# Kernel optimization log

Hardware: AMD Instinct MI355X
Metric: run time of the kernel (lower is better)

## Reference

```python
import jax, jax.numpy as jnp
import numpy as np

DIM = 256; HEADS = 8; HD = 32; WS = 3; LOCAL = WS * WS; SR = 4


def _unfold(x, ws):
    # x: (B, c, H, W) -> (B, c, ws*ws, H*W), zero padding (matches nn.Unfold)
    p = ws // 2
    B, c, H, W = x.shape
    xp = jnp.pad(x, ((0, 0), (0, 0), (p, p), (p, p)))
    pat = jnp.stack([xp[:, :, i:i + H, j:j + W] for i in range(ws) for j in range(ws)], axis=2)
    return pat.reshape(B, c, ws * ws, H * W)


def _l2norm(x):
    return x / jnp.sqrt(jnp.sum(x * x, axis=-1, keepdims=True) + 1e-12)


def setup_inputs():
    key = jax.random.key(0)
    ks = jax.random.split(key, 16)
    B, H, W, C, h, d = 4, 64, 64, DIM, HEADS, HD
    N = H * W; pH, pW = H // SR, W // SR; PL = pH * pW; L = 1024
    s = 0.02
    inp = {}
    inp["x"] = jax.random.normal(ks[0], (B, N, C), jnp.float32)
    inp["relative_coords_table"] = jax.random.uniform(ks[1], (L, 2), jnp.float32, -1.0, 1.0)
    inp["relative_pos_index"] = jax.random.randint(ks[2], (N, PL), 0, L)
    inp["q_w"] = jax.random.normal(ks[3], (C, C), jnp.float32) * s
    inp["q_b"] = jnp.zeros((C,), jnp.float32)
    inp["kv_w"] = jax.random.normal(ks[4], (C, 2 * C), jnp.float32) * s
    inp["kv_b"] = jnp.zeros((2 * C,), jnp.float32)
    inp["temperature"] = jnp.log(jnp.expm1(jnp.ones((h, 1, 1), jnp.float32) / 0.24))
    inp["query_embedding"] = jax.random.normal(ks[5], (h, 1, d), jnp.float32) * s
    inp["sr_w"] = jax.random.normal(ks[6], (C, C), jnp.float32) * s
    inp["sr_b"] = jnp.zeros((C,), jnp.float32)
    inp["norm_g"] = jnp.ones((C,), jnp.float32)
    inp["norm_b"] = jnp.zeros((C,), jnp.float32)
    inp["cpb1_w"] = jax.random.normal(ks[7], (2, 512), jnp.float32) * s
    inp["cpb1_b"] = jnp.zeros((512,), jnp.float32)
    inp["cpb2_w"] = jax.random.normal(ks[8], (512, h), jnp.float32) * s
    inp["cpb2_b"] = jnp.zeros((h,), jnp.float32)
    inp["rpb_local"] = jax.random.normal(ks[9], (h, LOCAL), jnp.float32) * 0.0004
    inp["learnable_tokens"] = jax.random.normal(ks[10], (h, d, LOCAL), jnp.float32) * s
    inp["learnable_bias"] = jnp.zeros((h, 1, LOCAL), jnp.float32)
    inp["proj_w"] = jax.random.normal(ks[11], (C, C), jnp.float32) * s
    inp["proj_b"] = jnp.zeros((C,), jnp.float32)
    inp["H"] = H
    inp["W"] = W
    return inp


def _forward(x, relative_coords_table, relative_pos_index, q_w, q_b, kv_w, kv_b,
             temperature, query_embedding, sr_w, sr_b, norm_g, norm_b,
             cpb1_w, cpb1_b, cpb2_w, cpb2_b, rpb_local, learnable_tokens,
             learnable_bias, proj_w, proj_b, H, W):
    B, N, C = x.shape
    h, d = HEADS, HD
    pH, pW = H // SR, W // SR
    PL = pH * pW

    # static buffers: per-pixel valid-neighbor count, log seq-length scale, padding mask
    uf1 = _unfold(jnp.ones((1, 1, H, W), jnp.float32), WS)[0, 0]   # (LOCAL, N)
    counts = uf1.sum(axis=0)[:, None]                               # (N, 1)
    seq_scale = jnp.log(counts + PL)                                # (N, 1)
    pad_mask = (uf1.T == 0)                                         # (N, LOCAL)

    q = (x @ q_w + q_b).reshape(B, N, h, d).transpose(0, 2, 1, 3)   # (B,h,N,d)
    q_norm = _l2norm(q)
    q_scaled = (q_norm + query_embedding) * jax.nn.softplus(temperature) * seq_scale

    kv = (x @ kv_w + kv_b).reshape(B, N, 2 * h, d).transpose(0, 2, 1, 3)
    k_local, v_local = kv[:, :h], kv[:, h:]                         # (B,h,N,d)

    # --- local branch: sliding-window QK^T + learned relative bias ---
    kn = _l2norm(k_local)
    k_img = kn.transpose(0, 1, 3, 2).reshape(B, h * d, H, W)
    k_uf = _unfold(k_img, WS).reshape(B, h, d, LOCAL, N)            # (B,h,d,l,N)
    attn_local = jnp.einsum('bhnd,bhdln->bhnl', q_scaled, k_uf) + rpb_local[None, :, None, :]
    attn_local = jnp.where(pad_mask[None, None], jnp.float32(-1e9), attn_local)

    # --- pooled global branch ---
    xs = jax.nn.gelu(x @ sr_w + sr_b, approximate=False)            # 1x1 conv + GELU
    xs = xs.reshape(B, pH, SR, pW, SR, C).mean(axis=(2, 4)).reshape(B, PL, C)
    mu = xs.mean(-1, keepdims=True)
    var = ((xs - mu) ** 2).mean(-1, keepdims=True)
    xs = (xs - mu) / jnp.sqrt(var + 1e-5) * norm_g + norm_b         # LayerNorm

    kvp = (xs @ kv_w + kv_b).reshape(B, PL, 2 * h, d).transpose(0, 2, 1, 3)
    k_pool, v_pool = kvp[:, :h], kvp[:, h:]
    kp = _l2norm(k_pool)

    # MLP-generated continuous relative position bias
    t = jax.nn.relu(relative_coords_table @ cpb1_w + cpb1_b) @ cpb2_w + cpb2_b  # (L,h)
    pool_bias = t.T[:, relative_pos_index.reshape(-1)].reshape(h, N, PL)

    attn_pool = jnp.einsum('bhnd,bhpd->bhnp', q_scaled, kp) + pool_bias[None]

    # joint softmax over [local | pool]
    attn = jax.nn.softmax(jnp.concatenate([attn_local, attn_pool], axis=-1), axis=-1)
    attn_local, attn_pool = attn[..., :LOCAL], attn[..., LOCAL:]

    # learnable-token refinement of local weights
    attn_local = jnp.einsum('bhnd,hdl->bhnl', q_norm, learnable_tokens) + learnable_bias[None] + attn_local

    v_img = v_local.transpose(0, 1, 3, 2).reshape(B, h * d, H, W)
    v_uf = _unfold(v_img, WS).reshape(B, h, d, LOCAL, N)            # zero-padded V
    x_local = jnp.einsum('bhnl,bhdln->bhnd', attn_local, v_uf)
    x_pool = jnp.einsum('bhnp,bhpd->bhnd', attn_pool, v_pool)

    out = (x_local + x_pool).transpose(0, 2, 1, 3).reshape(B, N, C)
    return out @ proj_w + proj_b


def reference(x, relative_coords_table, relative_pos_index, q_w, q_b, kv_w, kv_b,
              temperature, query_embedding, sr_w, sr_b, norm_g, norm_b,
              cpb1_w, cpb1_b, cpb2_w, cpb2_b, rpb_local, learnable_tokens,
              learnable_bias, proj_w, proj_b, H, W):
    return _forward(x, relative_coords_table, relative_pos_index, q_w, q_b, kv_w, kv_b,
                    temperature, query_embedding, sr_w, sr_b, norm_g, norm_b,
                    cpb1_w, cpb1_b, cpb2_w, cpb2_b, rpb_local, learnable_tokens,
                    learnable_bias, proj_w, proj_b, H, W)
```

## Files before the change

### kernel.cpp

```cpp
#include <hip/hip_runtime.h>
#include <math.h>

#define B_   4
#define N_   4096
#define C_   256
#define NH   8
#define D_   32
#define PL_  256
#define IMG  64

typedef __attribute__((ext_vector_type(8))) short short8b;
typedef __attribute__((ext_vector_type(4))) float f32x4;
typedef unsigned short ushort_t;

__device__ __forceinline__ ushort_t f2bf(float f) {
    unsigned u = __float_as_uint(f);
    u += 0x7FFFu + ((u >> 16) & 1u);
    return (ushort_t)(u >> 16);
}
__device__ __forceinline__ float bf2f(ushort_t s) {
    return __uint_as_float(((unsigned)s) << 16);
}
__device__ __forceinline__ unsigned pk2(float lo, float hi) {
    return (unsigned)f2bf(lo) | ((unsigned)f2bf(hi) << 16);
}
__device__ __forceinline__ float gelu_f(float v) {
    return 0.5f * v * (1.0f + erff(v * 0.70710678118654752440f));
}

__global__ __launch_bounds__(256) void prep_w(const float* __restrict__ x,
                                              const float* __restrict__ q_w,
                                              const float* __restrict__ kv_w,
                                              const float* __restrict__ sr_w,
                                              const float* __restrict__ p_w,
                                              ushort_t* __restrict__ x_bf,
                                              ushort_t* __restrict__ WTall,
                                              ushort_t* __restrict__ pwT)
{
    int gid = blockIdx.x * 256 + threadIdx.x;
    if (gid < 524288) {
        const float4* p = (const float4*)(x + (size_t)gid * 8);
        float4 v0 = p[0], v1 = p[1];
        short8b o;
        o[0]=(short)f2bf(v0.x); o[1]=(short)f2bf(v0.y);
        o[2]=(short)f2bf(v0.z); o[3]=(short)f2bf(v0.w);
        o[4]=(short)f2bf(v1.x); o[5]=(short)f2bf(v1.y);
        o[6]=(short)f2bf(v1.z); o[7]=(short)f2bf(v1.w);
        *(short8b*)&x_bf[(size_t)gid * 8] = o;
    } else {
        int wt = gid - 524288;
        int row = wt >> 5;
        int k0  = (wt & 31) << 3;
        const float* W; int N, n; ushort_t* dst;
        if (row < 256)       { W = q_w;  N = 256; n = row;        dst = WTall + (size_t)row * 256; }
        else if (row < 768)  { W = kv_w; N = 512; n = row - 256;  dst = WTall + (size_t)row * 256; }
        else if (row < 1024) { W = sr_w; N = 256; n = row - 768;  dst = WTall + (size_t)row * 256; }
        else                 { W = p_w;  N = 256; n = row - 1024; dst = pwT + (size_t)(row-1024) * 256; }
        short8b v;
        #pragma unroll
        for (int j = 0; j < 8; ++j) v[j] = (short)f2bf(W[(size_t)(k0 + j) * N + n]);
        *(short8b*)&dst[k0] = v;
    }
}

__global__ __launch_bounds__(256) void gemm_fused(const ushort_t* __restrict__ Abf,
                                                  const ushort_t* __restrict__ WTall,
                                                  const float* __restrict__ q_b,
                                                  const float* __restrict__ kv_b,
                                                  const float* __restrict__ sr_b,
                                                  float* __restrict__ buf_q,
                                                  float* __restrict__ buf_kv,
                                                  float* __restrict__ buf_sr)
{
    __shared__ __align__(16) ushort_t Bs[64 * 256];

    const int tid  = threadIdx.x;
    const int wv   = tid >> 6;
    const int lane = tid & 63;
    const int la   = lane & 15, lg = lane >> 4;
    const int m0   = blockIdx.y * 128 + wv * 32;
    const int bx   = blockIdx.x;
    const int n0   = bx * 64;

    {
        const int srow = tid >> 2, sm = tid & 3;
        const ushort_t* wrow = WTall + (size_t)(n0 + srow) * 256;
        #pragma unroll
        for (int c8 = 0; c8 < 8; ++c8) {
            int ck = c8 * 4 + sm;
            short8b v = *(const short8b*)&wrow[ck * 8];
            *(short8b*)&Bs[srow * 256 + ((ck ^ (srow & 3)) * 8)] = v;
        }
    }
    __syncthreads();

    const ushort_t* a0p = Abf + (size_t)(m0 + la) * 256 + lg * 8;
    const ushort_t* a1p = a0p + (size_t)16 * 256;

    f32x4 acc[2][4];
    #pragma unroll
    for (int i = 0; i < 2; ++i)
        #pragma unroll
        for (int j = 0; j < 4; ++j) acc[i][j] = (f32x4){0.f, 0.f, 0.f, 0.f};

    #pragma unroll
    for (int kit = 0; kit < 8; ++kit) {
        short8b a0 = *(const short8b*)(a0p + kit * 32);
        short8b a1 = *(const short8b*)(a1p + kit * 32);
        #pragma unroll
        for (int nf = 0; nf < 4; ++nf) {
            int brow = nf * 16 + la;
            short8b bb = *(const short8b*)&Bs[brow * 256 + (((kit*4 + lg) ^ (la & 3)) * 8)];
            acc[0][nf] = __builtin_amdgcn_mfma_f32_16x16x32_bf16(a0, bb, acc[0][nf], 0, 0, 0);
            acc[1][nf] = __builtin_amdgcn_mfma_f32_16x16x32_bf16(a1, bb, acc[1][nf], 0, 0, 0);
        }
    }

    float* outp; const float* bias; int base, stride; bool act;
    if (bx < 4)       { outp = buf_q;  bias = q_b;  base = 0;   stride = 256; act = false; }
    else if (bx < 12) { outp = buf_kv; bias = kv_b; base = 256; stride = 512; act = false; }
    else              { outp = buf_sr; bias = sr_b; base = 768; stride = 256; act = true;  }

    #pragma unroll
    for (int mf = 0; mf < 2; ++mf)
        #pragma unroll
        for (int nf = 0; nf < 4; ++nf)
            #pragma unroll
            for (int reg = 0; reg < 4; ++reg) {
                int m  = m0 + mf * 16 + lg * 4 + reg;
                int c  = n0 + nf * 16 + la - base;
                float v = acc[mf][nf][reg] + bias[c];
                if (act) v = gelu_f(v);
                outp[(size_t)m * stride + c] = v;
            }
}

template<int ACT>
__global__ __launch_bounds__(256) void gemm_mfma(const ushort_t* __restrict__ Abf,
                                                 const ushort_t* __restrict__ WT,
                                                 const float* __restrict__ bias,
                                                 float* __restrict__ out,
                                                 int M, int N)
{
    __shared__ __align__(16) ushort_t Bs[64 * 256];

    const int tid  = threadIdx.x;
    const int wv   = tid >> 6;
    const int lane = tid & 63;
    const int la   = lane & 15, lg = lane >> 4;
    const int m0   = blockIdx.y * 128 + wv * 32;
    const int n0   = blockIdx.x * 64;

    {
        const int srow = tid >> 2, sm = tid & 3;
        const ushort_t* wrow = WT + (size_t)(n0 + srow) * 256;
        #pragma unroll
        for (int c8 = 0; c8 < 8; ++c8) {
            int ck = c8 * 4 + sm;
            short8b v = *(const short8b*)&wrow[ck * 8];
            *(short8b*)&Bs[srow * 256 + ((ck ^ (srow & 3)) * 8)] = v;
        }
    }
    __syncthreads();

    const ushort_t* a0p = Abf + (size_t)(m0 + la) * 256 + lg * 8;
    const ushort_t* a1p = a0p + (size_t)16 * 256;

    f32x4 acc[2][4];
    #pragma unroll
    for (int i = 0; i < 2; ++i)
        #pragma unroll
        for (int j = 0; j < 4; ++j) acc[i][j] = (f32x4){0.f, 0.f, 0.f, 0.f};

    #pragma unroll
    for (int kit = 0; kit < 8; ++kit) {
        short8b a0 = *(const short8b*)(a0p + kit * 32);
        short8b a1 = *(const short8b*)(a1p + kit * 32);
        #pragma unroll
        for (int nf = 0; nf < 4; ++nf) {
            int brow = nf * 16 + la;
            short8b bb = *(const short8b*)&Bs[brow * 256 + (((kit*4 + lg) ^ (la & 3)) * 8)];
            acc[0][nf] = __builtin_amdgcn_mfma_f32_16x16x32_bf16(a0, bb, acc[0][nf], 0, 0, 0);
            acc[1][nf] = __builtin_amdgcn_mfma_f32_16x16x32_bf16(a1, bb, acc[1][nf], 0, 0, 0);
        }
    }
    #pragma unroll
    for (int mf = 0; mf < 2; ++mf)
        #pragma unroll
        for (int nf = 0; nf < 4; ++nf)
            #pragma unroll
            for (int reg = 0; reg < 4; ++reg) {
                int m  = m0 + mf * 16 + lg * 4 + reg;
                int nn = n0 + nf * 16 + la;
                float v = acc[mf][nf][reg] + bias[nn];
                if (ACT == 1) v = gelu_f(v);
                out[(size_t)m * N + nn] = v;
            }
}

__global__ __launch_bounds__(256) void qkn_prep(const float* __restrict__ buf_q,
                                                const float* __restrict__ buf_kv,
                                                const float* __restrict__ qe,
                                                const float* __restrict__ temp,
                                                ushort_t* __restrict__ qs_bf,
                                                ushort_t* __restrict__ knv_bf)
{
    int gid = blockIdx.x * 256 + threadIdx.x;
    int hh = gid & 7, bn = gid >> 3;
    int n = bn & (N_ - 1);
    {
        const float* src = buf_q + (size_t)bn * 256 + hh * 32;
        float qq[32]; float ss = 0.f;
        #pragma unroll
        for (int i = 0; i < 8; ++i) {
            float4 v = *(const float4*)&src[i*4];
            qq[i*4+0]=v.x; qq[i*4+1]=v.y; qq[i*4+2]=v.z; qq[i*4+3]=v.w;
            ss += v.x*v.x + v.y*v.y + v.z*v.z + v.w*v.w;
        }
        float inv = rsqrtf(ss + 1e-12f);
        float sp  = log1pf(expf(temp[hh]));
        int y = n >> 6, x = n & 63;
        int ci = 1 + (y > 0) + (y < IMG-1);
        int cj = 1 + (x > 0) + (x < IMG-1);
        float s2 = sp * logf((float)(ci*cj) + (float)PL_);
        ushort_t* dst = qs_bf + (size_t)bn * 256 + hh * 32;
        #pragma unroll
        for (int c = 0; c < 4; ++c) {
            short8b v;
            #pragma unroll
            for (int j = 0; j < 8; ++j)
                v[j] = (short)f2bf((qq[c*8+j]*inv + qe[hh*32 + c*8+j]) * s2);
            *(short8b*)&dst[c*8] = v;
        }
    }
    {
        const float* ksrc = buf_kv + (size_t)bn * 512 + hh * 32;
        float kk[32]; float ss = 0.f;
        #pragma unroll
        for (int i = 0; i < 8; ++i) {
            float4 v = *(const float4*)&ksrc[i*4];
            kk[i*4+0]=v.x; kk[i*4+1]=v.y; kk[i*4+2]=v.z; kk[i*4+3]=v.w;
            ss += v.x*v.x + v.y*v.y + v.z*v.z + v.w*v.w;
        }
        float inv = rsqrtf(ss + 1e-12f);
        ushort_t* kdst = knv_bf + (size_t)bn * 512 + hh * 32;
        #pragma unroll
        for (int c = 0; c < 4; ++c) {
            short8b v;
            #pragma unroll
            for (int j = 0; j < 8; ++j) v[j] = (short)f2bf(kk[c*8+j] * inv);
            *(short8b*)&kdst[c*8] = v;
        }
        const float* vsrc = ksrc + 256;
        ushort_t* vdst = kdst + 256;
        #pragma unroll
        for (int c = 0; c < 4; ++c) {
            short8b v;
            #pragma unroll
            for (int j = 0; j < 8; ++j) v[j] = (short)f2bf(vsrc[c*8+j]);
            *(short8b*)&vdst[c*8] = v;
        }
    }
}

__global__ __launch_bounds__(256) void vtrans_kernel(const ushort_t* __restrict__ knv,
                                                     ushort_t* __restrict__ vT)
{
    __shared__ __align__(16) ushort_t ts[256][40];
    int blk = blockIdx.x;
    int nt = blk & 15, bh = blk >> 4;
    int tid = threadIdx.x;
    const ushort_t* src = knv + ((size_t)((bh >> 3)*N_ + nt*256 + tid)) * 512 + 256 + (bh & 7)*32;
    #pragma unroll
    for (int c = 0; c < 4; ++c)
        *(short8b*)&ts[tid][c*8] = *(const short8b*)&src[c*8];
    __syncthreads();
    int d = tid >> 3, cc = tid & 7;
    ushort_t* dst = vT + ((size_t)bh*32 + d) * (size_t)N_ + nt*256;
    #pragma unroll
    for (int k = 0; k < 4; ++k) {
        int n0 = cc*32 + k*8;
        short8b v;
        #pragma unroll
        for (int j = 0; j < 8; ++j) v[j] = ts[n0+j][d];
        *(short8b*)&dst[n0] = v;
    }
}

__global__ __launch_bounds__(256) void kvp_prep(const float* __restrict__ buf_kvp,
                                                ushort_t* __restrict__ kp_bf,
                                                ushort_t* __restrict__ vpT_bf)
{
    int gid = blockIdx.x * 256 + threadIdx.x;
    if (gid >= B_ * PL_ * NH) return;
    int hh = gid & 7, bp = gid >> 3;
    int b = bp >> 8, p = bp & 255;
    const float* ksrc = buf_kvp + (size_t)bp * 512 + hh * 32;
    float kk[32]; float ss = 0.f;
    #pragma unroll
    for (int i = 0; i < 8; ++i) {
        float4 v = *(const float4*)&ksrc[i*4];
        kk[i*4+0]=v.x; kk[i*4+1]=v.y; kk[i*4+2]=v.z; kk[i*4+3]=v.w;
        ss += v.x*v.x + v.y*v.y + v.z*v.z + v.w*v.w;
    }
    float inv = rsqrtf(ss + 1e-12f);
    ushort_t* kdst = kp_bf + (((size_t)(b*NH + hh) * PL_) + p) * 32;
    #pragma unroll
    for (int c = 0; c < 4; ++c) {
        short8b v;
        #pragma unroll
        for (int j = 0; j < 8; ++j) v[j] = (short)f2bf(kk[c*8+j] * inv);
        *(short8b*)&kdst[c*8] = v;
    }
    const float* vsrc = ksrc + 256;
    ushort_t* vbase = vpT_bf + ((size_t)(b*NH + hh) * 32) * 256 + p;
    #pragma unroll
    for (int d = 0; d < 32; ++d) vbase[d * 256] = f2bf(vsrc[d]);
}

__global__ __launch_bounds__(256) void pool_ln_kernel(const float* __restrict__ sr,
                                                      const float* __restrict__ g,
                                                      const float* __restrict__ bb,
                                                      ushort_t* __restrict__ xs)
{
    __shared__ float red[256];
    int bp = blockIdx.x;
    int b = bp >> 8, p = bp & 255;
    int i0 = p >> 4, j0 = p & 15;
    int c = threadIdx.x;
    float s = 0.f;
    #pragma unroll
    for (int di = 0; di < 4; ++di)
        #pragma unroll
        for (int dj = 0; dj < 4; ++dj) {
            int n = (i0*4 + di) * IMG + (j0*4 + dj);
            s += sr[((size_t)b * N_ + n) * C_ + c];
        }
    s *= (1.f / 16.f);
    red[c] = s; __syncthreads();
    for (int o = 128; o > 0; o >>= 1) { if (c < o) red[c] += red[c+o]; __syncthreads(); }
    float mean = red[0] * (1.f/256.f);
    __syncthreads();
    float dcen = s - mean;
    red[c] = dcen * dcen; __syncthreads();
    for (int o = 128; o > 0; o >>= 1) { if (c < o) red[c] += red[c+o]; __syncthreads(); }
    float var = red[0] * (1.f/256.f);
    float outv = dcen * rsqrtf(var + 1e-5f) * g[c] + bb[c];
    xs[(size_t)bp * C_ + c] = f2bf(outv);
}

__global__ __launch_bounds__(64) void cpb_kernel(const float* __restrict__ rct,
                                                 const float* __restrict__ w1,
                                                 const float* __restrict__ b1,
                                                 const float* __restrict__ w2,
                                                 const float* __restrict__ b2,
                                                 float* __restrict__ tT)
{
    int l = blockIdx.x;
    int lane = threadIdx.x;
    float c0 = rct[l*2+0], c1 = rct[l*2+1];
    float acc[8] = {0,0,0,0,0,0,0,0};
    for (int j = lane; j < 512; j += 64) {
        float hv = fmaxf(c0 * w1[j] + c1 * w1[512+j] + b1[j], 0.f);
        #pragma unroll
        for (int hh = 0; hh < 8; ++hh) acc[hh] += hv * w2[j*8 + hh];
    }
    #pragma unroll
    for (int o = 32; o > 0; o >>= 1)
        #pragma unroll
        for (int hh = 0; hh < 8; ++hh) acc[hh] += __shfl_xor(acc[hh], o, 64);
    if (lane < 8) tT[lane * 1024 + l] = acc[lane] + b2[lane];
}

__global__ __launch_bounds__(256) void pb_kernel(const int* __restrict__ rpi,
                                                 const float* __restrict__ tT,
                                                 ushort_t* __restrict__ pbl)
{
    int gid = blockIdx.x * 256 + threadIdx.x;
    int la   = gid & 15;
    int lg   = (gid >> 4) & 3;
    int t    = (gid >> 6) & 15;
    int wv   = (gid >> 10) & 3;
    int tile = (gid >> 12) & 63;
    int h    = gid >> 18;
    int n  = tile * 64 + wv * 16 + la;
    int p0 = t * 16 + lg * 4;
    int4 r = *(const int4*)&rpi[(size_t)n * PL_ + p0];
    const float* tTh = tT + h * 1024;
    ushort4 o;
    o.x = f2bf(tTh[r.x]);
    o.y = f2bf(tTh[r.y]);
    o.z = f2bf(tTh[r.z]);
    o.w = f2bf(tTh[r.w]);
    *(ushort4*)&pbl[(size_t)gid * 4] = o;
}

__global__ __launch_bounds__(256) void attn_v4(
    const ushort_t* __restrict__ qs_g,
    const ushort_t* __restrict__ knv_g,
    const ushort_t* __restrict__ kp_g,
    const ushort_t* __restrict__ vpT_g,
    const ushort_t* __restrict__ vT_g,
    const ushort_t* __restrict__ pbl,
    const float* __restrict__ rpb,
    const float* __restrict__ qe,
    const float* __restrict__ temp,
    const float* __restrict__ lt,
    const float* __restrict__ lb,
    ushort_t* __restrict__ outp)
{
    __shared__ __align__(16) ushort_t qs_lds[64*32];
    __shared__ __align__(16) ushort_t ltT_lds[16*32];
    __shared__ __align__(16) ushort_t Wb_lds[4*3*16*40];
    __shared__ float wloc[64*10];
    __shared__ float wext[64*10];
    __shared__ float invs2[64];
    __shared__ float rpb_lds[9], elb_lds[9];

    const int tile = blockIdx.x;
    const int hh   = blockIdx.y;
    const int b    = blockIdx.z;
    const int tid  = threadIdx.x;
    const int wv   = tid >> 6;
    const int lane = tid & 63;
    const int la   = lane & 15;
    const int lg   = lane >> 4;
    const int r0   = wv * 16;

    {
        int row = tid >> 2, ck = tid & 3;
        short8b v = *(const short8b*)&qs_g[((size_t)(b*N_ + tile*64 + row)) * 256 + hh*32 + ck*8];
        *(short8b*)&qs_lds[row*32 + ((ck ^ (row & 3)) * 8)] = v;
    }
    {
        int l = tid >> 4, dd = (tid & 15) * 2;
        ushort_t a = (l < 9) ? f2bf(lt[hh*288 + dd*9 + l]) : (ushort_t)0;
        ushort_t c = (l < 9) ? f2bf(lt[hh*288 + (dd+1)*9 + l]) : (ushort_t)0;
        ltT_lds[l*32 + dd]   = a;
        ltT_lds[l*32 + dd+1] = c;
    }
    {
        short8b z = {0,0,0,0,0,0,0,0};
        for (int i = tid; i < 960; i += 256) *(short8b*)&Wb_lds[i*8] = z;
    }
    if (tid < 64) {
        int xx = tid;
        int ci = 1 + (tile > 0) + (tile < IMG-1);
        int cj = 1 + (xx > 0) + (xx < IMG-1);
        float sp = log1pf(expf(temp[hh]));
        invs2[tid] = 1.0f / (sp * logf((float)(ci*cj) + (float)PL_));
    }
    if (tid >= 64 && tid < 73) {
        int l = tid - 64;
        float e = 0.f;
        for (int d = 0; d < 32; ++d) e += qe[hh*32 + d] * lt[hh*288 + d*9 + l];
        elb_lds[l] = lb[hh*9 + l] - e;
        rpb_lds[l] = rpb[hh*9 + l];
    }
    __syncthreads();

    const short8b af = *(const short8b*)&qs_lds[(r0+la)*32 + ((lg ^ (la & 3)) * 8)];

    {
        f32x4 G[3][2];
        const f32x4 zc = {0.f,0.f,0.f,0.f};
        #pragma unroll
        for (int dyi = 0; dyi < 3; ++dyi) {
            int cy = tile + dyi - 1;
            cy = cy < 0 ? 0 : (cy > 63 ? 63 : cy);
            #pragma unroll
            for (int f = 0; f < 2; ++f) {
                int xp = wv*16 - 8 + 16*f + la;
                xp = xp < 0 ? 0 : (xp > 63 ? 63 : xp);
                const short8b kf = *(const short8b*)
                    &knv_g[((size_t)(b*N_ + cy*64 + xp)) * 512 + hh*32 + lg*8];
                G[dyi][f] = __builtin_amdgcn_mfma_f32_16x16x32_bf16(af, kf, zc, 0, 0, 0);
            }
        }
        #pragma unroll
        for (int f = 0; f < 2; ++f)
            #pragma unroll
            for (int reg = 0; reg < 4; ++reg) {
                int r  = lg*4 + reg;
                int dx = la + 16*f - 8 - r;
                if (dx >= -1 && dx <= 1) {
                    #pragma unroll
                    for (int dyi = 0; dyi < 3; ++dyi)
                        wloc[(r0 + r)*10 + dyi*3 + dx + 1] = G[dyi][f][reg];
                }
            }
    }

    {
        const short8b ltf = *(const short8b*)&ltT_lds[la*32 + lg*8];
        const f32x4 zc = {0.f,0.f,0.f,0.f};
        f32x4 E = __builtin_amdgcn_mfma_f32_16x16x32_bf16(af, ltf, zc, 0, 0, 0);
        if (la < 9) {
            #pragma unroll
            for (int reg = 0; reg < 4; ++reg) {
                int rr = r0 + lg*4 + reg;
                wext[rr*10 + la] = invs2[rr] * E[reg] + elb_lds[la];
            }
        }
    }

    const ushort_t* kph = kp_g + ((size_t)(b*NH + hh) * PL_) * 32;
    const ushort_t* pbw = pbl + ((((size_t)hh * 64 + tile) * 4 + wv) * 4096);

    f32x4 acc[16];
    #pragma unroll
    for (int t = 0; t < 16; ++t) {
        ushort4 b4 = *(const ushort4*)&pbw[t*256 + lg*64 + la*4];
        f32x4 c;
        c[0] = bf2f(b4.x); c[1] = bf2f(b4.y); c[2] = bf2f(b4.z); c[3] = bf2f(b4.w);
        short8b kf = *(const short8b*)&kph[(t*16 + la)*32 + lg*8];
        acc[t] = __builtin_amdgcn_mfma_f32_16x16x32_bf16(kf, af, c, 0, 0, 0);
    }

    const int rr = r0 + la;
    float mx = -3.0e38f;
    #pragma unroll
    for (int t = 0; t < 16; ++t)
        #pragma unroll
        for (int reg = 0; reg < 4; ++reg) mx = fmaxf(mx, acc[t][reg]);
    mx = fmaxf(mx, __shfl_xor(mx, 16, 64));
    mx = fmaxf(mx, __shfl_xor(mx, 32, 64));
    float lv[9];
    #pragma unroll
    for (int l = 0; l < 9; ++l) {
        int dy = l/3 - 1, dx = l%3 - 1;
        int yy = tile + dy, xx = rr + dx;
        bool val = (yy >= 0 && yy < IMG && xx >= 0 && xx < IMG);
        lv[l] = val ? (wloc[rr*10 + l] + rpb_lds[l]) : -1e9f;
        mx = fmaxf(mx, lv[l]);
    }

    float s = 0.f;
    #pragma unroll
    for (int t = 0; t < 16; ++t)
        #pragma unroll
        for (int reg = 0; reg < 4; ++reg) {
            float e = __expf(acc[t][reg] - mx);
            acc[t][reg] = e;
            s += e;
        }
    s += __shfl_xor(s, 16, 64);
    s += __shfl_xor(s, 32, 64);
    float sl = 0.f;
    float el[9];
    #pragma unroll
    for (int l = 0; l < 9; ++l) { el[l] = __expf(lv[l] - mx); sl += el[l]; }
    s += sl;
    const float inv = 1.f / s;

    if (lg == 0) {
        #pragma unroll
        for (int l = 0; l < 9; ++l) {
            int dy = l/3 - 1, dx = l%3 - 1;
            int yy = tile + dy, xx = rr + dx;
            bool val = (yy >= 0 && yy < IMG && xx >= 0 && xx < IMG);
            float wl = el[l]*inv + wext[rr*10 + l];
            Wb_lds[((wv*3 + l/3)*16 + la)*40 + (la + 8 + dx)] =
                val ? f2bf(wl) : (ushort_t)0;
        }
    }

    f32x4 o0 = {0.f,0.f,0.f,0.f}, o1 = {0.f,0.f,0.f,0.f};

    {
        const ushort_t* vTh = vT_g + (size_t)(b*NH + hh) * 32 * N_;
        #pragma unroll
        for (int dyi = 0; dyi < 3; ++dyi) {
            int cy = tile + dyi - 1;
            cy = cy < 0 ? 0 : (cy > 63 ? 63 : cy);
            int nb = cy*64 + wv*16 - 8 + lg*8;
            nb = nb < 0 ? 0 : (nb > (N_ - 8) ? (N_ - 8) : nb);
            short8b wf = *(const short8b*)&Wb_lds[((wv*3 + dyi)*16 + la)*40 + lg*8];
            short8b vf0 = *(const short8b*)&vTh[(size_t)la * N_ + nb];
            short8b vf1 = *(const short8b*)&vTh[(size_t)(16 + la) * N_ + nb];
            o0 = __builtin_amdgcn_mfma_f32_16x16x32_bf16(wf, vf0, o0, 0, 0, 0);
            o1 = __builtin_amdgcn_mfma_f32_16x16x32_bf16(wf, vf1, o1, 0, 0, 0);
        }
    }

    {
        const int src0 = la + 32*(lg & 1);
        const int src1 = src0 + 16;
        const bool hi  = (lg >= 2);
        const ushort_t* vph = vpT_g + ((size_t)(b*NH + hh) * 32) * 256;
        #pragma unroll
        for (int kk = 0; kk < 8; ++kk) {
            unsigned A0 = pk2(acc[2*kk][0]*inv,   acc[2*kk][1]*inv);
            unsigned A1 = pk2(acc[2*kk][2]*inv,   acc[2*kk][3]*inv);
            unsigned B0 = pk2(acc[2*kk+1][0]*inv, acc[2*kk+1][1]*inv);
            unsigned B1 = pk2(acc[2*kk+1][2]*inv, acc[2*kk+1][3]*inv);
            unsigned xa0 = __shfl(A0, src0, 64), xb0 = __shfl(B0, src0, 64);
            unsigned xa1 = __shfl(A1, src0, 64), xb1 = __shfl(B1, src0, 64);
            unsigned ya0 = __shfl(A0, src1, 64), yb0 = __shfl(B0, src1, 64);
            unsigned ya1 = __shfl(A1, src1, 64), yb1 = __shfl(B1, src1, 64);
            union { unsigned u[4]; short8b v; } wf;
            wf.u[0] = hi ? xb0 : xa0;
            wf.u[1] = hi ? xb1 : xa1;
            wf.u[2] = hi ? yb0 : ya0;
            wf.u[3] = hi ? yb1 : ya1;
            short8b vf0 = *(const short8b*)&vph[(size_t)la*256      + kk*32 + lg*8];
            short8b vf1 = *(const short8b*)&vph[(size_t)(16+la)*256 + kk*32 + lg*8];
            o0 = __builtin_amdgcn_mfma_f32_16x16x32_bf16(wf.v, vf0, o0, 0, 0, 0);
            o1 = __builtin_amdgcn_mfma_f32_16x16x32_bf16(wf.v, vf1, o1, 0, 0, 0);
        }
    }

    #pragma unroll
    for (int reg = 0; reg < 4; ++reg) {
        int r2 = r0 + lg*4 + reg;
        int n  = tile*64 + r2;
        ushort_t* orow = outp + ((size_t)(b*N_ + n)) * C_ + hh*32;
        orow[la]      = f2bf(o0[reg]);
        orow[16 + la] = f2bf(o1[reg]);
    }
}

extern "C" void kernel_launch(void* const* d_in, const int* in_sizes, int n_in,
                              void* d_out, int out_size, void* d_ws, size_t ws_size,
                              hipStream_t stream) {
    const float* x    = (const float*)d_in[0];
    const float* rct  = (const float*)d_in[1];
    const int*   rpi  = (const int*)  d_in[2];
    const float* q_w  = (const float*)d_in[3];
    const float* q_b  = (const float*)d_in[4];
    const float* kv_w = (const float*)d_in[5];
    const float* kv_b = (const float*)d_in[6];
    const float* temp = (const float*)d_in[7];
    const float* qe   = (const float*)d_in[8];
    const float* sr_w = (const float*)d_in[9];
    const float* sr_b = (const float*)d_in[10];
    const float* ng   = (const float*)d_in[11];
    const float* nb   = (const float*)d_in[12];
    const float* c1w  = (const float*)d_in[13];
    const float* c1b  = (const float*)d_in[14];
    const float* c2w  = (const float*)d_in[15];
    const float* c2b  = (const float*)d_in[16];
    const float* rpb  = (const float*)d_in[17];
    const float* lt   = (const float*)d_in[18];
    const float* lb   = (const float*)d_in[19];
    const float* p_w  = (const float*)d_in[20];
    const float* p_b  = (const float*)d_in[21];
    float* out = (float*)d_out;

    float* ws = (float*)d_ws;
    const size_t MN = (size_t)B_ * N_;
    float* buf_q   = ws;
    float* buf_kv  = buf_q   + MN * 256;
    float* buf_sr  = buf_kv  + MN * 512;
    float* buf_xs  = buf_sr  + MN * 256;
    float* buf_kvp = buf_xs  + (size_t)B_*PL_*256;
    float* buf_t   = buf_kvp + (size_t)B_*PL_*512;
    ushort_t* bf_base = (ushort_t*)(buf_t + 8*1024);
    ushort_t* x_bf   = bf_base;
    ushort_t* pre_bf = x_bf   + MN * 256;
    ushort_t* WTall  = pre_bf + MN * 256;
    ushort_t* pwT    = WTall  + 1024*256;
    ushort_t* qs_bf  = pwT    + 256*256;
    ushort_t* knv_bf = qs_bf  + MN * 256;
    ushort_t* kp_bf  = knv_bf + MN * 512;
    ushort_t* vpT_bf = kp_bf  + (size_t)B_*NH*PL_*32;
    ushort_t* xs_bf  = (ushort_t*)buf_xs;
    ushort_t* pbl    = (ushort_t*)buf_q;
    ushort_t* vT_bf  = (ushort_t*)buf_sr;

    const int M = (int)MN;

    prep_w<<<2208, 256, 0, stream>>>(x, q_w, kv_w, sr_w, p_w, x_bf, WTall, pwT);

    gemm_fused<<<dim3(16, M/128), 256, 0, stream>>>(x_bf, WTall, q_b, kv_b, sr_b,
                                                    buf_q, buf_kv, buf_sr);
    qkn_prep<<<(M * NH) / 256, 256, 0, stream>>>(buf_q, buf_kv, qe, temp, qs_bf, knv_bf);

    pool_ln_kernel<<<B_ * PL_, 256, 0, stream>>>(buf_sr, ng, nb, xs_bf);
    vtrans_kernel<<<B_ * NH * 16, 256, 0, stream>>>(knv_bf, vT_bf);

    gemm_mfma<0><<<dim3(8, (B_*PL_)/128), 256, 0, stream>>>(xs_bf, WTall + 256*256, kv_b,
                                                            buf_kvp, B_*PL_, 512);
    kvp_prep<<<(B_*PL_*NH + 255)/256, 256, 0, stream>>>(buf_kvp, kp_bf, vpT_bf);

    cpb_kernel<<<1024, 64, 0, stream>>>(rct, c1w, c1b, c2w, c2b, buf_t);
    pb_kernel<<<8192, 256, 0, stream>>>(rpi, buf_t, pbl);

    attn_v4<<<dim3(64, 8, 4), 256, 0, stream>>>(qs_bf, knv_bf, kp_bf, vpT_bf, vT_bf,
                                                pbl, rpb, qe, temp, lt, lb, pre_bf);

    gemm_mfma<0><<<dim3(4, M/128), 256, 0, stream>>>(pre_bf, pwT, p_b, out, M, 256);
}
```

Before: 161.0 us.

## Fuse q/k normalization into QKV GEMM epilogue and merge small prep kernels

The QKV GEMM epilogue now stages each tile in shared memory and performs per-head L2 normalization, scaling and bf16 conversion directly. This removes the fp32 q/kv intermediate buffers and the separate qkn_prep pass. The cpb MLP is folded into the weight-prep launch, and pos-bias gather, pool+layernorm and V transpose are merged into one mid_prep launch to cut launch count. In the attention kernel, the local-weight LDS staging buffer is replaced with register construction of the banded weight fragment, and s_setprio is added around the MFMA loops. The epilogue adds shared-memory traffic and extra barriers in the GEMM.

```diff
diff --git a/kernel.cpp b/kernel.cpp
--- a/kernel.cpp
+++ b/kernel.cpp
@@ -28,17 +28,25 @@
     return 0.5f * v * (1.0f + erff(v * 0.70710678118654752440f));
 }
 
-__global__ __launch_bounds__(256) void prep_w(const float* __restrict__ x,
-                                              const float* __restrict__ q_w,
-                                              const float* __restrict__ kv_w,
-                                              const float* __restrict__ sr_w,
-                                              const float* __restrict__ p_w,
-                                              ushort_t* __restrict__ x_bf,
-                                              ushort_t* __restrict__ WTall,
-                                              ushort_t* __restrict__ pwT)
+__global__ __launch_bounds__(256) void prep_all(const float* __restrict__ x,
+                                                const float* __restrict__ q_w,
+                                                const float* __restrict__ kv_w,
+                                                const float* __restrict__ sr_w,
+                                                const float* __restrict__ p_w,
+                                                const float* __restrict__ rct,
+                                                const float* __restrict__ c1w,
+                                                const float* __restrict__ c1b,
+                                                const float* __restrict__ c2w,
+                                                const float* __restrict__ c2b,
+                                                ushort_t* __restrict__ x_bf,
+                                                ushort_t* __restrict__ WTall,
+                                                ushort_t* __restrict__ pwT,
+                                                float* __restrict__ tT)
 {
-    int gid = blockIdx.x * 256 + threadIdx.x;
-    if (gid < 524288) {
+    const int blk = blockIdx.x;
+    const int tid = threadIdx.x;
+    if (blk < 2048) {
+        int gid = blk * 256 + tid;
         const float4* p = (const float4*)(x + (size_t)gid * 8);
         float4 v0 = p[0], v1 = p[1];
         short8b o;
@@ -47,8 +55,8 @@
         o[4]=(short)f2bf(v1.x); o[5]=(short)f2bf(v1.y);
         o[6]=(short)f2bf(v1.z); o[7]=(short)f2bf(v1.w);
         *(short8b*)&x_bf[(size_t)gid * 8] = o;
-    } else {
-        int wt = gid - 524288;
+    } else if (blk < 2208) {
+        int wt = (blk - 2048) * 256 + tid;
         int row = wt >> 5;
         int k0  = (wt & 31) << 3;
         const float* W; int N, n; ushort_t* dst;
@@ -60,6 +68,21 @@
         #pragma unroll
         for (int j = 0; j < 8; ++j) v[j] = (short)f2bf(W[(size_t)(k0 + j) * N + n]);
         *(short8b*)&dst[k0] = v;
+    } else {
+        int l = (blk - 2208) * 4 + (tid >> 6);
+        int lane = tid & 63;
+        float c0 = rct[l*2+0], c1 = rct[l*2+1];
+        float acc[8] = {0,0,0,0,0,0,0,0};
+        for (int j = lane; j < 512; j += 64) {
+            float hv = fmaxf(c0 * c1w[j] + c1 * c1w[512+j] + c1b[j], 0.f);
+            #pragma unroll
+            for (int hh = 0; hh < 8; ++hh) acc[hh] += hv * c2w[j*8 + hh];
+        }
+        #pragma unroll
+        for (int o = 32; o > 0; o >>= 1)
+            #pragma unroll
+            for (int hh = 0; hh < 8; ++hh) acc[hh] += __shfl_xor(acc[hh], o, 64);
+        if (lane < 8) tT[lane * 1024 + l] = acc[lane] + c2b[lane];
     }
 }
 
@@ -68,11 +91,15 @@
                                                   const float* __restrict__ q_b,
                                                   const float* __restrict__ kv_b,
                                                   const float* __restrict__ sr_b,
-                                                  float* __restrict__ buf_q,
-                                                  float* __restrict__ buf_kv,
+                                                  const float* __restrict__ temp,
+                                                  const float* __restrict__ qe,
+                                                  ushort_t* __restrict__ qs_bf,
+                                                  ushort_t* __restrict__ knv_bf,
                                                   float* __restrict__ buf_sr)
 {
-    __shared__ __align__(16) ushort_t Bs[64 * 256];
+    __shared__ __align__(16) unsigned char smem[128 * 68 * 4];
+    ushort_t* Bs = (ushort_t*)smem;
+    float*    Ep = (float*)smem;
 
     const int tid  = threadIdx.x;
     const int wv   = tid >> 6;
@@ -116,23 +143,84 @@
         }
     }
 
-    float* outp; const float* bias; int base, stride; bool act;
-    if (bx < 4)       { outp = buf_q;  bias = q_b;  base = 0;   stride = 256; act = false; }
-    else if (bx < 12) { outp = buf_kv; bias = kv_b; base = 256; stride = 512; act = false; }
-    else              { outp = buf_sr; bias = sr_b; base = 768; stride = 256; act = true;  }
-
-    #pragma unroll
-    for (int mf = 0; mf < 2; ++mf)
-        #pragma unroll
-        for (int nf = 0; nf < 4; ++nf)
-            #pragma unroll
-            for (int reg = 0; reg < 4; ++reg) {
-                int m  = m0 + mf * 16 + lg * 4 + reg;
-                int c  = n0 + nf * 16 + la - base;
-                float v = acc[mf][nf][reg] + bias[c];
-                if (act) v = gelu_f(v);
-                outp[(size_t)m * stride + c] = v;
-            }
+    if (bx < 12) {
+        const float* bias = (bx < 4) ? q_b : kv_b;
+        const int cb = (bx < 4) ? n0 : (n0 - 256);
+        __syncthreads();
+        #pragma unroll
+        for (int mf = 0; mf < 2; ++mf)
+            #pragma unroll
+            for (int nf = 0; nf < 4; ++nf)
+                #pragma unroll
+                for (int reg = 0; reg < 4; ++reg) {
+                    int rl = wv*32 + mf*16 + lg*4 + reg;
+                    int c  = nf*16 + la;
+                    Ep[rl*68 + c] = acc[mf][nf][reg] + bias[cb + c];
+                }
+        __syncthreads();
+        const int rl = tid >> 1, h2 = tid & 1;
+        const int m  = blockIdx.y * 128 + rl;
+        const float* rowp = &Ep[rl*68 + h2*32];
+        float vv[32]; float ss = 0.f;
+        #pragma unroll
+        for (int i = 0; i < 8; ++i) {
+            float4 v4 = *(const float4*)&rowp[i*4];
+            vv[i*4+0]=v4.x; vv[i*4+1]=v4.y; vv[i*4+2]=v4.z; vv[i*4+3]=v4.w;
+            ss += v4.x*v4.x + v4.y*v4.y + v4.z*v4.z + v4.w*v4.w;
+        }
+        if (bx < 4) {
+            int head = bx*2 + h2;
+            float inv = rsqrtf(ss + 1e-12f);
+            float sp  = log1pf(expf(temp[head]));
+            int n = m & (N_-1);
+            int y = n >> 6, xc = n & 63;
+            int ci = 1 + (y > 0) + (y < IMG-1);
+            int cj = 1 + (xc > 0) + (xc < IMG-1);
+            float s2 = sp * logf((float)(ci*cj) + (float)PL_);
+            ushort_t* dst = qs_bf + (size_t)m * 256 + head*32;
+            #pragma unroll
+            for (int c4 = 0; c4 < 4; ++c4) {
+                short8b o;
+                #pragma unroll
+                for (int j = 0; j < 8; ++j)
+                    o[j] = (short)f2bf((vv[c4*8+j]*inv + qe[head*32 + c4*8+j]) * s2);
+                *(short8b*)&dst[c4*8] = o;
+            }
+        } else if (bx < 8) {
+            int head = (bx-4)*2 + h2;
+            float inv = rsqrtf(ss + 1e-12f);
+            ushort_t* dst = knv_bf + (size_t)m * 512 + head*32;
+            #pragma unroll
+            for (int c4 = 0; c4 < 4; ++c4) {
+                short8b o;
+                #pragma unroll
+                for (int j = 0; j < 8; ++j) o[j] = (short)f2bf(vv[c4*8+j]*inv);
+                *(short8b*)&dst[c4*8] = o;
+            }
+        } else {
+            int head = (bx-8)*2 + h2;
+            ushort_t* dst = knv_bf + (size_t)m * 512 + 256 + head*32;
+            #pragma unroll
+            for (int c4 = 0; c4 < 4; ++c4) {
+                short8b o;
+                #pragma unroll
+                for (int j = 0; j < 8; ++j) o[j] = (short)f2bf(vv[c4*8+j]);
+                *(short8b*)&dst[c4*8] = o;
+            }
+        }
+    } else {
+        #pragma unroll
+        for (int mf = 0; mf < 2; ++mf)
+            #pragma unroll
+            for (int nf = 0; nf < 4; ++nf)
+                #pragma unroll
+                for (int reg = 0; reg < 4; ++reg) {
+                    int m = m0 + mf*16 + lg*4 + reg;
+                    int c = n0 + nf*16 + la - 768;
+                    float v = acc[mf][nf][reg] + sr_b[c];
+                    buf_sr[(size_t)m * 256 + c] = gelu_f(v);
+                }
+    }
 }
 
 template<int ACT>
@@ -198,92 +286,81 @@
             }
 }
 
-__global__ __launch_bounds__(256) void qkn_prep(const float* __restrict__ buf_q,
-                                                const float* __restrict__ buf_kv,
-                                                const float* __restrict__ qe,
-                                                const float* __restrict__ temp,
-                                                ushort_t* __restrict__ qs_bf,
-                                                ushort_t* __restrict__ knv_bf)
+__global__ __launch_bounds__(256) void mid_prep(const int* __restrict__ rpi,
+                                                const float* __restrict__ tT,
+                                                const ushort_t* __restrict__ knv,
+                                                const float* __restrict__ sr,
+                                                const float* __restrict__ g,
+                                                const float* __restrict__ bb,
+                                                ushort_t* __restrict__ pbl,
+                                                ushort_t* __restrict__ xs,
+                                                ushort_t* __restrict__ vT)
 {
-    int gid = blockIdx.x * 256 + threadIdx.x;
-    int hh = gid & 7, bn = gid >> 3;
-    int n = bn & (N_ - 1);
-    {
-        const float* src = buf_q + (size_t)bn * 256 + hh * 32;
-        float qq[32]; float ss = 0.f;
-        #pragma unroll
-        for (int i = 0; i < 8; ++i) {
-            float4 v = *(const float4*)&src[i*4];
-            qq[i*4+0]=v.x; qq[i*4+1]=v.y; qq[i*4+2]=v.z; qq[i*4+3]=v.w;
-            ss += v.x*v.x + v.y*v.y + v.z*v.z + v.w*v.w;
-        }
-        float inv = rsqrtf(ss + 1e-12f);
-        float sp  = log1pf(expf(temp[hh]));
-        int y = n >> 6, x = n & 63;
-        int ci = 1 + (y > 0) + (y < IMG-1);
-        int cj = 1 + (x > 0) + (x < IMG-1);
-        float s2 = sp * logf((float)(ci*cj) + (float)PL_);
-        ushort_t* dst = qs_bf + (size_t)bn * 256 + hh * 32;
-        #pragma unroll
-        for (int c = 0; c < 4; ++c) {
+    __shared__ float red[256];
+    __shared__ __align__(16) ushort_t ts[256][40];
+    const int blk = blockIdx.x;
+    const int tid = threadIdx.x;
+
+    if (blk < 8192) {
+        int gid = blk * 256 + tid;
+        int la   = gid & 15;
+        int lg   = (gid >> 4) & 3;
+        int t    = (gid >> 6) & 15;
+        int wv   = (gid >> 10) & 3;
+        int tile = (gid >> 12) & 63;
+        int h    = gid >> 18;
+        int n  = tile * 64 + wv * 16 + la;
+        int p0 = t * 16 + lg * 4;
+        int4 r = *(const int4*)&rpi[(size_t)n * PL_ + p0];
+        const float* tTh = tT + h * 1024;
+        ushort4 o;
+        o.x = f2bf(tTh[r.x]);
+        o.y = f2bf(tTh[r.y]);
+        o.z = f2bf(tTh[r.z]);
+        o.w = f2bf(tTh[r.w]);
+        *(ushort4*)&pbl[(size_t)gid * 4] = o;
+    } else if (blk < 9216) {
+        int bp = blk - 8192;
+        int b = bp >> 8, p = bp & 255;
+        int i0 = p >> 4, j0 = p & 15;
+        int c = tid;
+        float s = 0.f;
+        #pragma unroll
+        for (int di = 0; di < 4; ++di)
+            #pragma unroll
+            for (int dj = 0; dj < 4; ++dj) {
+                int n = (i0*4 + di) * IMG + (j0*4 + dj);
+                s += sr[((size_t)b * N_ + n) * C_ + c];
+            }
+        s *= (1.f / 16.f);
+        red[c] = s; __syncthreads();
+        for (int o = 128; o > 0; o >>= 1) { if (c < o) red[c] += red[c+o]; __syncthreads(); }
+        float mean = red[0] * (1.f/256.f);
+        __syncthreads();
+        float dcen = s - mean;
+        red[c] = dcen * dcen; __syncthreads();
+        for (int o = 128; o > 0; o >>= 1) { if (c < o) red[c] += red[c+o]; __syncthreads(); }
+        float var = red[0] * (1.f/256.f);
+        float outv = dcen * rsqrtf(var + 1e-5f) * g[c] + bb[c];
+        xs[(size_t)bp * C_ + c] = f2bf(outv);
+    } else {
+        int vb = blk - 9216;
+        int nt = vb & 15, bh = vb >> 4;
+        const ushort_t* src = knv + ((size_t)((bh >> 3)*N_ + nt*256 + tid)) * 512 + 256 + (bh & 7)*32;
+        #pragma unroll
+        for (int c = 0; c < 4; ++c)
+            *(short8b*)&ts[tid][c*8] = *(const short8b*)&src[c*8];
+        __syncthreads();
+        int d = tid >> 3, cc = tid & 7;
+        ushort_t* dst = vT + ((size_t)bh*32 + d) * (size_t)N_ + nt*256;
+        #pragma unroll
+        for (int k = 0; k < 4; ++k) {
+            int n0 = cc*32 + k*8;
             short8b v;
             #pragma unroll
-            for (int j = 0; j < 8; ++j)
-                v[j] = (short)f2bf((qq[c*8+j]*inv + qe[hh*32 + c*8+j]) * s2);
-            *(short8b*)&dst[c*8] = v;
-        }
-    }
-    {
-        const float* ksrc = buf_kv + (size_t)bn * 512 + hh * 32;
-        float kk[32]; float ss = 0.f;
-        #pragma unroll
-        for (int i = 0; i < 8; ++i) {
-            float4 v = *(const float4*)&ksrc[i*4];
-            kk[i*4+0]=v.x; kk[i*4+1]=v.y; kk[i*4+2]=v.z; kk[i*4+3]=v.w;
-            ss += v.x*v.x + v.y*v.y + v.z*v.z + v.w*v.w;
-        }
-        float inv = rsqrtf(ss + 1e-12f);
-        ushort_t* kdst = knv_bf + (size_t)bn * 512 + hh * 32;
-        #pragma unroll
-        for (int c = 0; c < 4; ++c) {
-            short8b v;
-            #pragma unroll
-            for (int j = 0; j < 8; ++j) v[j] = (short)f2bf(kk[c*8+j] * inv);
-            *(short8b*)&kdst[c*8] = v;
-        }
-        const float* vsrc = ksrc + 256;
-        ushort_t* vdst = kdst + 256;
-        #pragma unroll
-        for (int c = 0; c < 4; ++c) {
-            short8b v;
-            #pragma unroll
-            for (int j = 0; j < 8; ++j) v[j] = (short)f2bf(vsrc[c*8+j]);
-            *(short8b*)&vdst[c*8] = v;
-        }
-    }
-}
-
-__global__ __launch_bounds__(256) void vtrans_kernel(const ushort_t* __restrict__ knv,
-                                                     ushort_t* __restrict__ vT)
-{
-    __shared__ __align__(16) ushort_t ts[256][40];
-    int blk = blockIdx.x;
-    int nt = blk & 15, bh = blk >> 4;
-    int tid = threadIdx.x;
-    const ushort_t* src = knv + ((size_t)((bh >> 3)*N_ + nt*256 + tid)) * 512 + 256 + (bh & 7)*32;
-    #pragma unroll
-    for (int c = 0; c < 4; ++c)
-        *(short8b*)&ts[tid][c*8] = *(const short8b*)&src[c*8];
-    __syncthreads();
-    int d = tid >> 3, cc = tid & 7;
-    ushort_t* dst = vT + ((size_t)bh*32 + d) * (size_t)N_ + nt*256;
-    #pragma unroll
-    for (int k = 0; k < 4; ++k) {
-        int n0 = cc*32 + k*8;
-        short8b v;
-        #pragma unroll
-        for (int j = 0; j < 8; ++j) v[j] = ts[n0+j][d];
-        *(short8b*)&dst[n0] = v;
+            for (int j = 0; j < 8; ++j) v[j] = ts[n0+j][d];
+            *(short8b*)&dst[n0] = v;
+        }
     }
 }
 
@@ -318,84 +395,7 @@
     for (int d = 0; d < 32; ++d) vbase[d * 256] = f2bf(vsrc[d]);
 }
 
-__global__ __launch_bounds__(256) void pool_ln_kernel(const float* __restrict__ sr,
-                                                      const float* __restrict__ g,
-                                                      const float* __restrict__ bb,
-                                                      ushort_t* __restrict__ xs)
-{
-    __shared__ float red[256];
-    int bp = blockIdx.x;
-    int b = bp >> 8, p = bp & 255;
-    int i0 = p >> 4, j0 = p & 15;
-    int c = threadIdx.x;
-    float s = 0.f;
-    #pragma unroll
-    for (int di = 0; di < 4; ++di)
-        #pragma unroll
-        for (int dj = 0; dj < 4; ++dj) {
-            int n = (i0*4 + di) * IMG + (j0*4 + dj);
-            s += sr[((size_t)b * N_ + n) * C_ + c];
-        }
-    s *= (1.f / 16.f);
-    red[c] = s; __syncthreads();
-    for (int o = 128; o > 0; o >>= 1) { if (c < o) red[c] += red[c+o]; __syncthreads(); }
-    float mean = red[0] * (1.f/256.f);
-    __syncthreads();
-    float dcen = s - mean;
-    red[c] = dcen * dcen; __syncthreads();
-    for (int o = 128; o > 0; o >>= 1) { if (c < o) red[c] += red[c+o]; __syncthreads(); }
-    float var = red[0] * (1.f/256.f);
-    float outv = dcen * rsqrtf(var + 1e-5f) * g[c] + bb[c];
-    xs[(size_t)bp * C_ + c] = f2bf(outv);
-}
-
-__global__ __launch_bounds__(64) void cpb_kernel(const float* __restrict__ rct,
-                                                 const float* __restrict__ w1,
-                                                 const float* __restrict__ b1,
-                                                 const float* __restrict__ w2,
-                                                 const float* __restrict__ b2,
-                                                 float* __restrict__ tT)
-{
-    int l = blockIdx.x;
-    int lane = threadIdx.x;
-    float c0 = rct[l*2+0], c1 = rct[l*2+1];
-    float acc[8] = {0,0,0,0,0,0,0,0};
-    for (int j = lane; j < 512; j += 64) {
-        float hv = fmaxf(c0 * w1[j] + c1 * w1[512+j] + b1[j], 0.f);
-        #pragma unroll
-        for (int hh = 0; hh < 8; ++hh) acc[hh] += hv * w2[j*8 + hh];
-    }
-    #pragma unroll
-    for (int o = 32; o > 0; o >>= 1)
-        #pragma unroll
-        for (int hh = 0; hh < 8; ++hh) acc[hh] += __shfl_xor(acc[hh], o, 64);
-    if (lane < 8) tT[lane * 1024 + l] = acc[lane] + b2[lane];
-}
-
-__global__ __launch_bounds__(256) void pb_kernel(const int* __restrict__ rpi,
-                                                 const float* __restrict__ tT,
-                                                 ushort_t* __restrict__ pbl)
-{
-    int gid = blockIdx.x * 256 + threadIdx.x;
-    int la   = gid & 15;
-    int lg   = (gid >> 4) & 3;
-    int t    = (gid >> 6) & 15;
-    int wv   = (gid >> 10) & 3;
-    int tile = (gid >> 12) & 63;
-    int h    = gid >> 18;
-    int n  = tile * 64 + wv * 16 + la;
-    int p0 = t * 16 + lg * 4;
-    int4 r = *(const int4*)&rpi[(size_t)n * PL_ + p0];
-    const float* tTh = tT + h * 1024;
-    ushort4 o;
-    o.x = f2bf(tTh[r.x]);
-    o.y = f2bf(tTh[r.y]);
-    o.z = f2bf(tTh[r.z]);
-    o.w = f2bf(tTh[r.w]);
-    *(ushort4*)&pbl[(size_t)gid * 4] = o;
-}
-
-__global__ __launch_bounds__(256) void attn_v4(
+__global__ __launch_bounds__(256) void attn_v5(
     const ushort_t* __restrict__ qs_g,
     const ushort_t* __restrict__ knv_g,
     const ushort_t* __restrict__ kp_g,
@@ -411,7 +411,6 @@
 {
     __shared__ __align__(16) ushort_t qs_lds[64*32];
     __shared__ __align__(16) ushort_t ltT_lds[16*32];
-    __shared__ __align__(16) ushort_t Wb_lds[4*3*16*40];
     __shared__ float wloc[64*10];
     __shared__ float wext[64*10];
     __shared__ float invs2[64];
@@ -439,10 +438,6 @@
         ltT_lds[l*32 + dd]   = a;
         ltT_lds[l*32 + dd+1] = c;
     }
-    {
-        short8b z = {0,0,0,0,0,0,0,0};
-        for (int i = tid; i < 960; i += 256) *(short8b*)&Wb_lds[i*8] = z;
-    }
     if (tid < 64) {
         int xx = tid;
         int ci = 1 + (tile > 0) + (tile < IMG-1);
@@ -508,6 +503,7 @@
     const ushort_t* pbw = pbl + ((((size_t)hh * 64 + tile) * 4 + wv) * 4096);
 
     f32x4 acc[16];
+    __builtin_amdgcn_s_setprio(1);
     #pragma unroll
     for (int t = 0; t < 16; ++t) {
         ushort4 b4 = *(const ushort4*)&pbw[t*256 + lg*64 + la*4];
@@ -516,6 +512,7 @@
         short8b kf = *(const short8b*)&kph[(t*16 + la)*32 + lg*8];
         acc[t] = __builtin_amdgcn_mfma_f32_16x16x32_bf16(kf, af, c, 0, 0, 0);
     }
+    __builtin_amdgcn_s_setprio(0);
 
     const int rr = r0 + la;
     float mx = -3.0e38f;
@@ -553,33 +550,42 @@
     s += sl;
     const float inv = 1.f / s;
 
-    if (lg == 0) {
-        #pragma unroll
-        for (int l = 0; l < 9; ++l) {
-            int dy = l/3 - 1, dx = l%3 - 1;
-            int yy = tile + dy, xx = rr + dx;
-            bool val = (yy >= 0 && yy < IMG && xx >= 0 && xx < IMG);
-            float wl = el[l]*inv + wext[rr*10 + l];
-            Wb_lds[((wv*3 + l/3)*16 + la)*40 + (la + 8 + dx)] =
-                val ? f2bf(wl) : (ushort_t)0;
-        }
+    ushort_t b9[9];
+    #pragma unroll
+    for (int l = 0; l < 9; ++l) {
+        int dy = l/3 - 1, dx = l%3 - 1;
+        int yy = tile + dy, xx = rr + dx;
+        bool val = (yy >= 0 && yy < IMG && xx >= 0 && xx < IMG);
+        float wl = el[l]*inv + wext[rr*10 + l];
+        b9[l] = val ? f2bf(wl) : (ushort_t)0;
     }
 
     f32x4 o0 = {0.f,0.f,0.f,0.f}, o1 = {0.f,0.f,0.f,0.f};
 
+    __builtin_amdgcn_s_setprio(1);
     {
         const ushort_t* vTh = vT_g + (size_t)(b*NH + hh) * 32 * N_;
         #pragma unroll
         for (int dyi = 0; dyi < 3; ++dyi) {
             int cy = tile + dyi - 1;
             cy = cy < 0 ? 0 : (cy > 63 ? 63 : cy);
-            int nb = cy*64 + wv*16 - 8 + lg*8;
+            int nb = cy*64 + r0 - 8 + lg*8;
             nb = nb < 0 ? 0 : (nb > (N_ - 8) ? (N_ - 8) : nb);
-            short8b wf = *(const short8b*)&Wb_lds[((wv*3 + dyi)*16 + la)*40 + lg*8];
+            union { ushort_t us[8]; short8b v; } wf;
+            #pragma unroll
+            for (int j = 0; j < 8; ++j) {
+                int c  = lg*8 + j;
+                int dx = c - la - 8;
+                ushort_t w = 0;
+                if (dx == -1) w = b9[dyi*3 + 0];
+                if (dx ==  0) w = b9[dyi*3 + 1];
+                if (dx ==  1) w = b9[dyi*3 + 2];
+                wf.us[j] = w;
+            }
             short8b vf0 = *(const short8b*)&vTh[(size_t)la * N_ + nb];
             short8b vf1 = *(const short8b*)&vTh[(size_t)(16 + la) * N_ + nb];
-            o0 = __builtin_amdgcn_mfma_f32_16x16x32_bf16(wf, vf0, o0, 0, 0, 0);
-            o1 = __builtin_amdgcn_mfma_f32_16x16x32_bf16(wf, vf1, o1, 0, 0, 0);
+            o0 = __builtin_amdgcn_mfma_f32_16x16x32_bf16(wf.v, vf0, o0, 0, 0, 0);
+            o1 = __builtin_amdgcn_mfma_f32_16x16x32_bf16(wf.v, vf1, o1, 0, 0, 0);
         }
     }
 
@@ -609,6 +615,7 @@
             o1 = __builtin_amdgcn_mfma_f32_16x16x32_bf16(wf.v, vf1, o1, 0, 0, 0);
         }
     }
+    __builtin_amdgcn_s_setprio(0);
 
     #pragma unroll
     for (int reg = 0; reg < 4; ++reg) {
@@ -649,14 +656,10 @@
 
     float* ws = (float*)d_ws;
     const size_t MN = (size_t)B_ * N_;
-    float* buf_q   = ws;
-    float* buf_kv  = buf_q   + MN * 256;
-    float* buf_sr  = buf_kv  + MN * 512;
-    float* buf_xs  = buf_sr  + MN * 256;
-    float* buf_kvp = buf_xs  + (size_t)B_*PL_*256;
+    float* buf_sr  = ws;
+    float* buf_kvp = buf_sr + MN * 256;
     float* buf_t   = buf_kvp + (size_t)B_*PL_*512;
-    ushort_t* bf_base = (ushort_t*)(buf_t + 8*1024);
-    ushort_t* x_bf   = bf_base;
+    ushort_t* x_bf   = (ushort_t*)(buf_t + 8*1024);
     ushort_t* pre_bf = x_bf   + MN * 256;
     ushort_t* WTall  = pre_bf + MN * 256;
     ushort_t* pwT    = WTall  + 1024*256;
@@ -664,30 +667,22 @@
     ushort_t* knv_bf = qs_bf  + MN * 256;
     ushort_t* kp_bf  = knv_bf + MN * 512;
     ushort_t* vpT_bf = kp_bf  + (size_t)B_*NH*PL_*32;
-    ushort_t* xs_bf  = (ushort_t*)buf_xs;
-    ushort_t* pbl    = (ushort_t*)buf_q;
-    ushort_t* vT_bf  = (ushort_t*)buf_sr;
+    ushort_t* vT_bf  = vpT_bf + (size_t)B_*NH*32*PL_;
+    ushort_t* pbl    = vT_bf  + (size_t)B_*NH*32*N_;
+    ushort_t* xs_bf  = pbl    + (size_t)2097152*4;
 
     const int M = (int)MN;
 
-    prep_w<<<2208, 256, 0, stream>>>(x, q_w, kv_w, sr_w, p_w, x_bf, WTall, pwT);
-
+    prep_all<<<2464, 256, 0, stream>>>(x, q_w, kv_w, sr_w, p_w, rct,
+                                       c1w, c1b, c2w, c2b, x_bf, WTall, pwT, buf_t);
     gemm_fused<<<dim3(16, M/128), 256, 0, stream>>>(x_bf, WTall, q_b, kv_b, sr_b,
-                                                    buf_q, buf_kv, buf_sr);
-    qkn_prep<<<(M * NH) / 256, 256, 0, stream>>>(buf_q, buf_kv, qe, temp, qs_bf, knv_bf);
-
-    pool_ln_kernel<<<B_ * PL_, 256, 0, stream>>>(buf_sr, ng, nb, xs_bf);
-    vtrans_kernel<<<B_ * NH * 16, 256, 0, stream>>>(knv_bf, vT_bf);
-
-    gemm_mfma<0><<<dim3(8, (B_*PL_)/128), 256, 0, stream>>>(xs_bf, WTall + 256*256, kv_b,
-                                                            buf_kvp, B_*PL_, 512);
+                                                    temp, qe, qs_bf, knv_bf, buf_sr);
+    mid_prep<<<9728, 256, 0, stream>>>(rpi, buf_t, knv_bf, buf_sr, ng, nb,
+                                       pbl, xs_bf, vT_bf);
+    gemm_mfma<0><<<dim3(8, 8), 256, 0, stream>>>(xs_bf, WTall + 256*256, kv_b,
+                                                 buf_kvp, B_*PL_, 512);
     kvp_prep<<<(B_*PL_*NH + 255)/256, 256, 0, stream>>>(buf_kvp, kp_bf, vpT_bf);
-
-    cpb_kernel<<<1024, 64, 0, stream>>>(rct, c1w, c1b, c2w, c2b, buf_t);
-    pb_kernel<<<8192, 256, 0, stream>>>(rpi, buf_t, pbl);
-
-    attn_v4<<<dim3(64, 8, 4), 256, 0, stream>>>(qs_bf, knv_bf, kp_bf, vpT_bf, vT_bf,
+    attn_v5<<<dim3(64, 8, 4), 256, 0, stream>>>(qs_bf, knv_bf, kp_bf, vpT_bf, vT_bf,
                                                 pbl, rpb, qe, temp, lt, lb, pre_bf);
-
     gemm_mfma<0><<<dim3(4, M/128), 256, 0, stream>>>(pre_bf, pwT, p_b, out, M, 256);
 }
```

Result: faster. 155.1 us (-3.7%).
